# Kernel tuning notes

Measured on AMD Instinct MI355X. Metric: run time of the kernel, lower is better.

Reference implementation:

```python
import jax, jax.numpy as jnp
import numpy as np
import math

MAXL = 5
TAUS = [16, 16, 16, 16, 16, 16]
BATCH = 256


def _fact(n):
    return math.factorial(n)


def _cg(l1, l2, l, m1, m2):
    # Standard Clebsch-Gordan coefficient <l1 m1; l2 m2 | l (m1+m2)> (Condon-Shortley)
    m = m1 + m2
    if abs(m) > l or l < abs(l1 - l2) or l > l1 + l2:
        return 0.0
    pref = (2 * l + 1) * _fact(l + l1 - l2) * _fact(l - l1 + l2) * _fact(l1 + l2 - l) / _fact(l1 + l2 + l + 1)
    pref *= _fact(l + m) * _fact(l - m) * _fact(l1 - m1) * _fact(l1 + m1) * _fact(l2 - m2) * _fact(l2 + m2)
    kmin = max(0, -(l - l2 + m1), -(l - l1 - m2))
    kmax = min(l1 + l2 - l, l1 - m1, l2 + m2)
    s = 0.0
    for k in range(kmin, kmax + 1):
        s += ((-1) ** k) / (_fact(k) * _fact(l1 + l2 - l - k) * _fact(l1 - m1 - k)
                            * _fact(l2 + m2 - k) * _fact(l - l2 + m1 + k) * _fact(l - l1 - m2 + k))
    return math.sqrt(pref) * s


def _cg_table(l1, l2, l):
    C = np.zeros((2 * l1 + 1, 2 * l2 + 1, 2 * l + 1), dtype=np.float32)
    for m1 in range(-l1, l1 + 1):
        for m2 in range(-l2, l2 + 1):
            m = m1 + m2
            if abs(m) <= l:
                C[m1 + l1, m2 + l2, m + l] = _cg(l1, l2, l, m1, m2)
    return jnp.asarray(C)


# triples in the exact CUDA-kernel loop order (defines fragment ordering per output l)
_TRIPLES = [(l1, l2, l)
            for l1 in range(MAXL + 1)
            for l2 in range(l1 + 1)
            for l in range(l1 - l2, min(l1 + l2, MAXL) + 1)]
_CG_TABLES = {t: _cg_table(*t) for t in _TRIPLES}


def setup_inputs() -> dict:
    key = jax.random.key(0)
    inp = {}
    for l in range(MAXL + 1):
        key, k = jax.random.split(key)
        inp[f"act{l}"] = jax.random.normal(k, (BATCH, TAUS[l], 2 * l + 1, 2), dtype=jnp.float32)
    return inp


def _cg_forward(acts):
    B = acts[0].shape[0]
    outs = [[] for _ in range(MAXL + 1)]
    for (l1, l2, l) in _TRIPLES:
        C = _CG_TABLES[(l1, l2, l)]  # (2l1+1, 2l2+1, 2l+1)
        A1, A2 = acts[l1], acts[l2]  # (B, tau, 2l*+1, 2) complex as real pairs
        x1, y1 = A1[..., 0], A1[..., 1]
        x2, y2 = A2[..., 0], A2[..., 1]
        # complex outer product of channels, contracted against CG coefficients
        rr = jnp.einsum('bip,bjq,pqm->bijm', x1, x2, C)
        ii = jnp.einsum('bip,bjq,pqm->bijm', y1, y2, C)
        ri = jnp.einsum('bip,bjq,pqm->bijm', x1, y2, C)
        ir = jnp.einsum('bip,bjq,pqm->bijm', y1, x2, C)
        frag = jnp.stack([rr - ii, ri + ir], axis=-1)  # (B, tau1, tau2, 2l+1, 2)
        outs[l].append(frag.reshape(B, -1, 2 * l + 1, 2))
    # per output l: concatenate fragments along channel dim in loop order
    return tuple(jnp.concatenate(fr, axis=1) for fr in outs)


def reference(act0, act1, act2, act3, act4, act5):
    return _cg_forward([act0, act1, act2, act3, act4, act5])
```

## Files before the change

### kernel.cpp

```cpp
#include <hip/hip_runtime.h>


constexpr double CFACT[17] = {
    1.0, 1.0, 2.0, 6.0, 24.0, 120.0, 720.0, 5040.0, 40320.0, 362880.0,
    3628800.0, 39916800.0, 479001600.0, 6227020800.0, 87178291200.0,
    1307674368000.0, 20922789888000.0};

constexpr double csqrt_ce(double x) {
    double g = x > 1.0 ? x : 1.0;
    for (int i = 0; i < 60; ++i) g = 0.5 * (g + x / g);
    return g;
}

constexpr double cg_ce(int l1, int l2, int l, int m1, int m2) {
    int m = m1 + m2;
    if (m > l || -m > l || l < l1 - l2 || l > l1 + l2) return 0.0;
    double pref = (double)(2 * l + 1) * CFACT[l + l1 - l2] * CFACT[l - l1 + l2] *
                  CFACT[l1 + l2 - l] / CFACT[l1 + l2 + l + 1];
    pref *= CFACT[l + m] * CFACT[l - m] * CFACT[l1 - m1] * CFACT[l1 + m1] *
            CFACT[l2 - m2] * CFACT[l2 + m2];
    int kmin = 0;
    if (-(l - l2 + m1) > kmin) kmin = -(l - l2 + m1);
    if (-(l - l1 - m2) > kmin) kmin = -(l - l1 - m2);
    int kmax = l1 + l2 - l;
    if (l1 - m1 < kmax) kmax = l1 - m1;
    if (l2 + m2 < kmax) kmax = l2 + m2;
    double s = 0.0;
    for (int k = kmin; k <= kmax; ++k) {
        double d = CFACT[k] * CFACT[l1 + l2 - l - k] * CFACT[l1 - m1 - k] *
                   CFACT[l2 + m2 - k] * CFACT[l - l2 + m1 + k] * CFACT[l - l1 - m2 + k];
        s += ((k & 1) ? -1.0 : 1.0) / d;
    }
    return csqrt_ce(pref) * s;
}

constexpr int OUT_BASE[6]  = {0, 786432, 4718592, 13238272, 26083328, 42598400};
constexpr int STRIDE_B[6]  = {3072, 15360, 33280, 50176, 64512, 67584};

constexpr int PL1[21] = {5,5,4,4,5,3,4,3,5,2,4,5,3,2,1,5,4,3,2,1,0};
constexpr int PL2[21] = {5,4,4,3,3,3,2,2,2,2,1,1,1,1,1,0,0,0,0,0,0};
constexpr int PFRAG[21][6] = {
    { 5,  9, 12, 13, 13, 11},
    {-1,  8, 11, 12, 12, 10},
    { 4,  7,  9,  9,  8,  5},
    {-1,  6,  8,  8,  7,  4},
    {-1, -1, 10, 11, 11,  9},
    { 3,  5,  6,  5,  3,  1},
    {-1, -1,  7,  7,  6,  3},
    {-1,  4,  5,  4,  2,  0},
    {-1, -1, -1, 10, 10,  8},
    { 2,  3,  3,  1,  0, -1},
    {-1, -1, -1,  6,  5,  2},
    {-1, -1, -1, -1,  9,  7},
    {-1, -1,  4,  3,  1, -1},
    {-1,  2,  2,  0, -1, -1},
    { 1,  1,  0, -1, -1, -1},
    {-1, -1, -1, -1, -1,  6},
    {-1, -1, -1, -1,  4, -1},
    {-1, -1, -1,  2, -1, -1},
    {-1, -1,  1, -1, -1, -1},
    {-1,  0, -1, -1, -1, -1},
    { 0, -1, -1, -1, -1, -1},
};


template <int L1, int L2, int P, int Q, int LV>
__device__ __forceinline__ void accum_l(float wr, float wi, float* ar, float* ai) {
    constexpr int LMIN = L1 - L2;
    constexpr int LMAX = (L1 + L2 < 5) ? (L1 + L2) : 5;
    constexpr int M  = (P - L1) + (Q - L2);
    constexpr int AM = M < 0 ? -M : M;
    if constexpr (AM <= LV) {
        constexpr float c = (float)cg_ce(L1, L2, LV, P - L1, Q - L2);
        if constexpr (c != 0.0f) {
            constexpr int idx = LV * LV - LMIN * LMIN + M + LV;
            ar[idx] += c * wr;
            ai[idx] += c * wi;
        }
    }
    if constexpr (LV < LMAX) accum_l<L1, L2, P, Q, LV + 1>(wr, wi, ar, ai);
}

template <int L1, int L2, int P, int Q>
__device__ __forceinline__ void do_q(const float2* z1, const float2* z2,
                                     float* ar, float* ai) {
    float wr = z1[P].x * z2[Q].x - z1[P].y * z2[Q].y;
    float wi = z1[P].x * z2[Q].y + z1[P].y * z2[Q].x;
    accum_l<L1, L2, P, Q, L1 - L2>(wr, wi, ar, ai);
    if constexpr (Q + 1 < 2 * L2 + 1) do_q<L1, L2, P, Q + 1>(z1, z2, ar, ai);
}

template <int L1, int L2, int P>
__device__ __forceinline__ void do_p(const float2* z1, const float2* z2,
                                     float* ar, float* ai) {
    do_q<L1, L2, P, 0>(z1, z2, ar, ai);
    if constexpr (P + 1 < 2 * L1 + 1) do_p<L1, L2, P + 1>(z1, z2, ar, ai);
}

template <int PAIR>
__device__ __forceinline__ void pair_body(const float* const acts[6],
                                          float* __restrict__ out,
                                          int b, int tid, float* stage) {
    constexpr int L1   = PL1[PAIR];
    constexpr int L2   = PL2[PAIR];
    constexpr int LMIN = L1 - L2;
    constexpr int LMAX = (L1 + L2 < 5) ? (L1 + L2) : 5;
    constexpr int N1   = 2 * L1 + 1;
    constexpr int N2   = 2 * L2 + 1;
    constexpr int NTOT = (LMAX + 1) * (LMAX + 1) - LMIN * LMIN;
    constexpr int LST  = (LMIN == 0) ? 1 : LMIN;

    const int i = tid >> 4;
    const int j = tid & 15;
    const int wave = tid >> 6;
    const int lane = tid & 63;

    const float2* __restrict__ z1p =
        (const float2*)(acts[L1] + (size_t)(b * 16 + i) * N1 * 2);
    const float2* __restrict__ z2p =
        (const float2*)(acts[L2] + (size_t)(b * 16 + j) * N2 * 2);
    float2 z1[N1], z2[N2];
#pragma unroll
    for (int p = 0; p < N1; ++p) z1[p] = z1p[p];
#pragma unroll
    for (int q = 0; q < N2; ++q) z2[q] = z2p[q];

    float ar[NTOT], ai[NTOT];
#pragma unroll
    for (int k = 0; k < NTOT; ++k) { ar[k] = 0.f; ai[k] = 0.f; }

    do_p<L1, L2, 0>(z1, z2, ar, ai);

    float* const wbuf = stage + (size_t)wave * 2816;
#pragma unroll
    for (int l = LMIN; l <= LMAX; ++l) {
        const int NM   = 2 * l + 1;
        const int off  = l * l - LMIN * LMIN;
        const int frag = PFRAG[PAIR][l];
        if (NM == 1) {
            float2* __restrict__ d2 = (float2*)(out + OUT_BASE[l] +
                (size_t)b * STRIDE_B[l] + (size_t)frag * 512);
            d2[tid] = make_float2(ar[off], ai[off]);
        } else {
            float* sb = wbuf + (size_t)((l - LST) & 1) * 1408;
            float2* st = (float2*)sb + lane * NM;
#pragma unroll
            for (int k = 0; k < NM; ++k) st[k] = make_float2(ar[off + k], ai[off + k]);
            asm volatile("s_waitcnt lgkmcnt(0)" ::: "memory");
            const float4* __restrict__ s4 = (const float4*)sb;
            float4* __restrict__ d4 = (float4*)(out + OUT_BASE[l] +
                (size_t)b * STRIDE_B[l] + (size_t)frag * 512 * NM) +
                (size_t)wave * 32 * NM;
            const int cnt = 32 * NM;
#pragma unroll
            for (int k = lane; k < cnt; k += 64) d4[k] = s4[k];
        }
    }
}

__global__ __launch_bounds__(256, 3) void fCG_kernel(
    const float* __restrict__ a0, const float* __restrict__ a1,
    const float* __restrict__ a2, const float* __restrict__ a3,
    const float* __restrict__ a4, const float* __restrict__ a5,
    float* __restrict__ out) {
    __shared__ __align__(16) float stage[4 * 2816];
    const float* acts[6] = {a0, a1, a2, a3, a4, a5};
    int pair = blockIdx.x >> 8;
    int b    = blockIdx.x & 255;
    int tid  = threadIdx.x;
    switch (pair) {
        case 0:  pair_body<0>(acts, out, b, tid, stage); break;
        case 1:  pair_body<1>(acts, out, b, tid, stage); break;
        case 2:  pair_body<2>(acts, out, b, tid, stage); break;
        case 3:  pair_body<3>(acts, out, b, tid, stage); break;
        case 4:  pair_body<4>(acts, out, b, tid, stage); break;
        case 5:  pair_body<5>(acts, out, b, tid, stage); break;
        case 6:  pair_body<6>(acts, out, b, tid, stage); break;
        case 7:  pair_body<7>(acts, out, b, tid, stage); break;
        case 8:  pair_body<8>(acts, out, b, tid, stage); break;
        case 9:  pair_body<9>(acts, out, b, tid, stage); break;
        case 10: pair_body<10>(acts, out, b, tid, stage); break;
        case 11: pair_body<11>(acts, out, b, tid, stage); break;
        case 12: pair_body<12>(acts, out, b, tid, stage); break;
        case 13: pair_body<13>(acts, out, b, tid, stage); break;
        case 14: pair_body<14>(acts, out, b, tid, stage); break;
        case 15: pair_body<15>(acts, out, b, tid, stage); break;
        case 16: pair_body<16>(acts, out, b, tid, stage); break;
        case 17: pair_body<17>(acts, out, b, tid, stage); break;
        case 18: pair_body<18>(acts, out, b, tid, stage); break;
        case 19: pair_body<19>(acts, out, b, tid, stage); break;
        case 20: pair_body<20>(acts, out, b, tid, stage); break;
        default: break;
    }
}

extern "C" void kernel_launch(void* const* d_in, const int* in_sizes, int n_in,
                              void* d_out, int out_size, void* d_ws, size_t ws_size,
                              hipStream_t stream) {
    const float* a0 = (const float*)d_in[0];
    const float* a1 = (const float*)d_in[1];
    const float* a2 = (const float*)d_in[2];
    const float* a3 = (const float*)d_in[3];
    const float* a4 = (const float*)d_in[4];
    const float* a5 = (const float*)d_in[5];
    float* out = (float*)d_out;
    fCG_kernel<<<dim3(21 * 256), dim3(256), 0, stream>>>(a0, a1, a2, a3, a4, a5, out);
}
```

Baseline: 269.4 us.

## Process multiple batches per block with per-pair chunk sizes to balance work

Each block now loops over several batch elements of one (l1,l2) pair instead of handling a single one. Heavy pairs take 2 batches per block and light pairs take 4 or 8, so the grid shrinks from 5376 to 1376 blocks and per-block work is more even. This cuts block launch and scheduling overhead and amortises setup. The cost is less parallelism, a serial loop inside each block, and a linear scan over BBASE to find the pair. Reusing the same LDS staging buffer across iterations may also add hazards between waves.

```diff
diff --git a/kernel.cpp b/kernel.cpp
--- a/kernel.cpp
+++ b/kernel.cpp
@@ -63,6 +63,12 @@
     { 0, -1, -1, -1, -1, -1},
 };
 
+constexpr int CHUNK[21] = {2,2,2,2,2, 4,4,4,4,4,4,4, 8,8,8,8,8,8,8,8,8};
+constexpr int BBASE[22] = {0,128,256,384,512,640,
+                           704,768,832,896,960,1024,1088,
+                           1120,1152,1184,1216,1248,1280,1312,1344,1376};
+constexpr int NBLOCKS = 1376;
+
 
 template <int L1, int L2, int P, int Q, int LV>
 __device__ __forceinline__ void accum_l(float wr, float wi, float* ar, float* ai) {
@@ -158,6 +164,16 @@
     }
 }
 
+template <int PAIR>
+__device__ __forceinline__ void pair_loop(const float* const acts[6],
+                                          float* __restrict__ out,
+                                          int blk, int tid, float* stage) {
+    const int b0 = (blk - BBASE[PAIR]) * CHUNK[PAIR];
+#pragma unroll 1
+    for (int bb = 0; bb < CHUNK[PAIR]; ++bb)
+        pair_body<PAIR>(acts, out, b0 + bb, tid, stage);
+}
+
 __global__ __launch_bounds__(256, 3) void fCG_kernel(
     const float* __restrict__ a0, const float* __restrict__ a1,
     const float* __restrict__ a2, const float* __restrict__ a3,
@@ -165,31 +181,32 @@
     float* __restrict__ out) {
     __shared__ __align__(16) float stage[4 * 2816];
     const float* acts[6] = {a0, a1, a2, a3, a4, a5};
-    int pair = blockIdx.x >> 8;
-    int b    = blockIdx.x & 255;
-    int tid  = threadIdx.x;
+    const int blk = blockIdx.x;
+    const int tid = threadIdx.x;
+    int pair = 0;
+    while (pair < 20 && blk >= BBASE[pair + 1]) ++pair;
     switch (pair) {
-        case 0:  pair_body<0>(acts, out, b, tid, stage); break;
-        case 1:  pair_body<1>(acts, out, b, tid, stage); break;
-        case 2:  pair_body<2>(acts, out, b, tid, stage); break;
-        case 3:  pair_body<3>(acts, out, b, tid, stage); break;
-        case 4:  pair_body<4>(acts, out, b, tid, stage); break;
-        case 5:  pair_body<5>(acts, out, b, tid, stage); break;
-        case 6:  pair_body<6>(acts, out, b, tid, stage); break;
-        case 7:  pair_body<7>(acts, out, b, tid, stage); break;
-        case 8:  pair_body<8>(acts, out, b, tid, stage); break;
-        case 9:  pair_body<9>(acts, out, b, tid, stage); break;
-        case 10: pair_body<10>(acts, out, b, tid, stage); break;
-        case 11: pair_body<11>(acts, out, b, tid, stage); break;
-        case 12: pair_body<12>(acts, out, b, tid, stage); break;
-        case 13: pair_body<13>(acts, out, b, tid, stage); break;
-        case 14: pair_body<14>(acts, out, b, tid, stage); break;
-        case 15: pair_body<15>(acts, out, b, tid, stage); break;
-        case 16: pair_body<16>(acts, out, b, tid, stage); break;
-        case 17: pair_body<17>(acts, out, b, tid, stage); break;
-        case 18: pair_body<18>(acts, out, b, tid, stage); break;
-        case 19: pair_body<19>(acts, out, b, tid, stage); break;
-        case 20: pair_body<20>(acts, out, b, tid, stage); break;
+        case 0:  pair_loop<0>(acts, out, blk, tid, stage); break;
+        case 1:  pair_loop<1>(acts, out, blk, tid, stage); break;
+        case 2:  pair_loop<2>(acts, out, blk, tid, stage); break;
+        case 3:  pair_loop<3>(acts, out, blk, tid, stage); break;
+        case 4:  pair_loop<4>(acts, out, blk, tid, stage); break;
+        case 5:  pair_loop<5>(acts, out, blk, tid, stage); break;
+        case 6:  pair_loop<6>(acts, out, blk, tid, stage); break;
+        case 7:  pair_loop<7>(acts, out, blk, tid, stage); break;
+        case 8:  pair_loop<8>(acts, out, blk, tid, stage); break;
+        case 9:  pair_loop<9>(acts, out, blk, tid, stage); break;
+        case 10: pair_loop<10>(acts, out, blk, tid, stage); break;
+        case 11: pair_loop<11>(acts, out, blk, tid, stage); break;
+        case 12: pair_loop<12>(acts, out, blk, tid, stage); break;
+        case 13: pair_loop<13>(acts, out, blk, tid, stage); break;
+        case 14: pair_loop<14>(acts, out, blk, tid, stage); break;
+        case 15: pair_loop<15>(acts, out, blk, tid, stage); break;
+        case 16: pair_loop<16>(acts, out, blk, tid, stage); break;
+        case 17: pair_loop<17>(acts, out, blk, tid, stage); break;
+        case 18: pair_loop<18>(acts, out, blk, tid, stage); break;
+        case 19: pair_loop<19>(acts, out, blk, tid, stage); break;
+        case 20: pair_loop<20>(acts, out, blk, tid, stage); break;
         default: break;
     }
 }
@@ -204,5 +221,5 @@
     const float* a4 = (const float*)d_in[4];
     const float* a5 = (const float*)d_in[5];
     float* out = (float*)d_out;
-    fCG_kernel<<<dim3(21 * 256), dim3(256), 0, stream>>>(a0, a1, a2, a3, a4, a5, out);
-}
+    fCG_kernel<<<dim3(NBLOCKS), dim3(256), 0, stream>>>(a0, a1, a2, a3, a4, a5, out);
+}
```

Measured after the change: 283.2 us. +5.1%, slower.

## Split large-pair accumulation into two l-range passes to cut register pressure

Applied to the files above, without the earlier changes.

For pairs whose accumulator count exceeds 20 per component, the output l range is split into two balanced chunks, each recomputing the complex products but holding only half the accumulators in registers. The LDS staging buffer is halved to a single buffer per wave, with an extra waitcnt added before reuse, and launch bounds are raised from 3 to 4 blocks per CU. The aim is higher occupancy and less spilling, at the cost of reloading the inputs and recomputing the products for the split pairs.

```diff
diff --git a/kernel.cpp b/kernel.cpp
--- a/kernel.cpp
+++ b/kernel.cpp
@@ -63,38 +63,106 @@
     { 0, -1, -1, -1, -1, -1},
 };
 
-
-template <int L1, int L2, int P, int Q, int LV>
+constexpr int split_l(int lmin, int lmax) {
+    int ntot = (lmax + 1) * (lmax + 1) - lmin * lmin;
+    if (ntot <= 20) return lmax;
+    int best = lmin, bestm = 1 << 30;
+    for (int s = lmin; s < lmax; ++s) {
+        int front = (s + 1) * (s + 1) - lmin * lmin;
+        int back  = ntot - front;
+        int mx = front > back ? front : back;
+        if (mx < bestm) { bestm = mx; best = s; }
+    }
+    return best;
+}
+
+
+template <int L1, int L2, int P, int Q, int LV, int LLO, int LHI>
 __device__ __forceinline__ void accum_l(float wr, float wi, float* ar, float* ai) {
-    constexpr int LMIN = L1 - L2;
-    constexpr int LMAX = (L1 + L2 < 5) ? (L1 + L2) : 5;
     constexpr int M  = (P - L1) + (Q - L2);
     constexpr int AM = M < 0 ? -M : M;
     if constexpr (AM <= LV) {
         constexpr float c = (float)cg_ce(L1, L2, LV, P - L1, Q - L2);
         if constexpr (c != 0.0f) {
-            constexpr int idx = LV * LV - LMIN * LMIN + M + LV;
+            constexpr int idx = LV * LV - LLO * LLO + M + LV;
             ar[idx] += c * wr;
             ai[idx] += c * wi;
         }
     }
-    if constexpr (LV < LMAX) accum_l<L1, L2, P, Q, LV + 1>(wr, wi, ar, ai);
-}
-
-template <int L1, int L2, int P, int Q>
+    if constexpr (LV < LHI) accum_l<L1, L2, P, Q, LV + 1, LLO, LHI>(wr, wi, ar, ai);
+}
+
+template <int L1, int L2, int P, int Q, int LLO, int LHI>
 __device__ __forceinline__ void do_q(const float2* z1, const float2* z2,
                                      float* ar, float* ai) {
     float wr = z1[P].x * z2[Q].x - z1[P].y * z2[Q].y;
     float wi = z1[P].x * z2[Q].y + z1[P].y * z2[Q].x;
-    accum_l<L1, L2, P, Q, L1 - L2>(wr, wi, ar, ai);
-    if constexpr (Q + 1 < 2 * L2 + 1) do_q<L1, L2, P, Q + 1>(z1, z2, ar, ai);
-}
-
-template <int L1, int L2, int P>
+    accum_l<L1, L2, P, Q, LLO, LLO, LHI>(wr, wi, ar, ai);
+    if constexpr (Q + 1 < 2 * L2 + 1) do_q<L1, L2, P, Q + 1, LLO, LHI>(z1, z2, ar, ai);
+}
+
+template <int L1, int L2, int P, int LLO, int LHI>
 __device__ __forceinline__ void do_p(const float2* z1, const float2* z2,
                                      float* ar, float* ai) {
-    do_q<L1, L2, P, 0>(z1, z2, ar, ai);
-    if constexpr (P + 1 < 2 * L1 + 1) do_p<L1, L2, P + 1>(z1, z2, ar, ai);
+    do_q<L1, L2, P, 0, LLO, LHI>(z1, z2, ar, ai);
+    if constexpr (P + 1 < 2 * L1 + 1) do_p<L1, L2, P + 1, LLO, LHI>(z1, z2, ar, ai);
+}
+
+template <int PAIR, int LLO, int LHI>
+__device__ __forceinline__ void pair_chunk(const float* const acts[6],
+                                           float* __restrict__ out,
+                                           int b, int tid, float* wbuf) {
+    constexpr int L1   = PL1[PAIR];
+    constexpr int L2   = PL2[PAIR];
+    constexpr int N1   = 2 * L1 + 1;
+    constexpr int N2   = 2 * L2 + 1;
+    constexpr int NTOT = (LHI + 1) * (LHI + 1) - LLO * LLO;
+
+    const int i = tid >> 4;
+    const int j = tid & 15;
+    const int wave = tid >> 6;
+    const int lane = tid & 63;
+
+    const float2* __restrict__ z1p =
+        (const float2*)(acts[L1] + (size_t)(b * 16 + i) * N1 * 2);
+    const float2* __restrict__ z2p =
+        (const float2*)(acts[L2] + (size_t)(b * 16 + j) * N2 * 2);
+    float2 z1[N1], z2[N2];
+#pragma unroll
+    for (int p = 0; p < N1; ++p) z1[p] = z1p[p];
+#pragma unroll
+    for (int q = 0; q < N2; ++q) z2[q] = z2p[q];
+
+    float ar[NTOT], ai[NTOT];
+#pragma unroll
+    for (int k = 0; k < NTOT; ++k) { ar[k] = 0.f; ai[k] = 0.f; }
+
+    do_p<L1, L2, 0, LLO, LHI>(z1, z2, ar, ai);
+
+#pragma unroll
+    for (int l = LLO; l <= LHI; ++l) {
+        const int NM   = 2 * l + 1;
+        const int off  = l * l - LLO * LLO;
+        const int frag = PFRAG[PAIR][l];
+        if (NM == 1) {
+            float2* __restrict__ d2 = (float2*)(out + OUT_BASE[l] +
+                (size_t)b * STRIDE_B[l] + (size_t)frag * 512);
+            d2[tid] = make_float2(ar[off], ai[off]);
+        } else {
+            asm volatile("s_waitcnt lgkmcnt(0)" ::: "memory");
+            float2* st = (float2*)wbuf + lane * NM;
+#pragma unroll
+            for (int k = 0; k < NM; ++k) st[k] = make_float2(ar[off + k], ai[off + k]);
+            asm volatile("s_waitcnt lgkmcnt(0)" ::: "memory");
+            const float4* __restrict__ s4 = (const float4*)wbuf;
+            float4* __restrict__ d4 = (float4*)(out + OUT_BASE[l] +
+                (size_t)b * STRIDE_B[l] + (size_t)frag * 512 * NM) +
+                (size_t)wave * 32 * NM;
+            const int cnt = 32 * NM;
+#pragma unroll
+            for (int k = lane; k < cnt; k += 64) d4[k] = s4[k];
+        }
+    }
 }
 
 template <int PAIR>
@@ -105,65 +173,19 @@
     constexpr int L2   = PL2[PAIR];
     constexpr int LMIN = L1 - L2;
     constexpr int LMAX = (L1 + L2 < 5) ? (L1 + L2) : 5;
-    constexpr int N1   = 2 * L1 + 1;
-    constexpr int N2   = 2 * L2 + 1;
-    constexpr int NTOT = (LMAX + 1) * (LMAX + 1) - LMIN * LMIN;
-    constexpr int LST  = (LMIN == 0) ? 1 : LMIN;
-
-    const int i = tid >> 4;
-    const int j = tid & 15;
-    const int wave = tid >> 6;
-    const int lane = tid & 63;
-
-    const float2* __restrict__ z1p =
-        (const float2*)(acts[L1] + (size_t)(b * 16 + i) * N1 * 2);
-    const float2* __restrict__ z2p =
-        (const float2*)(acts[L2] + (size_t)(b * 16 + j) * N2 * 2);
-    float2 z1[N1], z2[N2];
-#pragma unroll
-    for (int p = 0; p < N1; ++p) z1[p] = z1p[p];
-#pragma unroll
-    for (int q = 0; q < N2; ++q) z2[q] = z2p[q];
-
-    float ar[NTOT], ai[NTOT];
-#pragma unroll
-    for (int k = 0; k < NTOT; ++k) { ar[k] = 0.f; ai[k] = 0.f; }
-
-    do_p<L1, L2, 0>(z1, z2, ar, ai);
-
-    float* const wbuf = stage + (size_t)wave * 2816;
-#pragma unroll
-    for (int l = LMIN; l <= LMAX; ++l) {
-        const int NM   = 2 * l + 1;
-        const int off  = l * l - LMIN * LMIN;
-        const int frag = PFRAG[PAIR][l];
-        if (NM == 1) {
-            float2* __restrict__ d2 = (float2*)(out + OUT_BASE[l] +
-                (size_t)b * STRIDE_B[l] + (size_t)frag * 512);
-            d2[tid] = make_float2(ar[off], ai[off]);
-        } else {
-            float* sb = wbuf + (size_t)((l - LST) & 1) * 1408;
-            float2* st = (float2*)sb + lane * NM;
-#pragma unroll
-            for (int k = 0; k < NM; ++k) st[k] = make_float2(ar[off + k], ai[off + k]);
-            asm volatile("s_waitcnt lgkmcnt(0)" ::: "memory");
-            const float4* __restrict__ s4 = (const float4*)sb;
-            float4* __restrict__ d4 = (float4*)(out + OUT_BASE[l] +
-                (size_t)b * STRIDE_B[l] + (size_t)frag * 512 * NM) +
-                (size_t)wave * 32 * NM;
-            const int cnt = 32 * NM;
-#pragma unroll
-            for (int k = lane; k < cnt; k += 64) d4[k] = s4[k];
-        }
-    }
-}
-
-__global__ __launch_bounds__(256, 3) void fCG_kernel(
+    constexpr int S    = split_l(LMIN, LMAX);
+    float* const wbuf = stage + (size_t)(tid >> 6) * 1408;
+    pair_chunk<PAIR, LMIN, S>(acts, out, b, tid, wbuf);
+    if constexpr (S < LMAX)
+        pair_chunk<PAIR, S + 1, LMAX>(acts, out, b, tid, wbuf);
+}
+
+__global__ __launch_bounds__(256, 4) void fCG_kernel(
     const float* __restrict__ a0, const float* __restrict__ a1,
     const float* __restrict__ a2, const float* __restrict__ a3,
     const float* __restrict__ a4, const float* __restrict__ a5,
     float* __restrict__ out) {
-    __shared__ __align__(16) float stage[4 * 2816];
+    __shared__ __align__(16) float stage[4 * 1408];
     const float* acts[6] = {a0, a1, a2, a3, a4, a5};
     int pair = blockIdx.x >> 8;
     int b    = blockIdx.x & 255;
```

New measurement: 295.0 us. 1.09x slower.
